# Performance work log

Hardware: AMD Instinct MI355X
Metric: run time of the kernel (lower is better)

## Reference

```python
import jax, jax.numpy as jnp
import numpy as np

ATTEN_SIZE = 5  # half-window; module-global atten_size in source (0 there is non-functional)
B, S, D_IN, HID, OUT = 8, 2048, 512, 512, 2


def _xavier(key, shape):
    fan_in, fan_out = shape
    std = (2.0 / (fan_in + fan_out)) ** 0.5
    return jax.random.normal(key, shape, dtype=jnp.float32) * std


def setup_inputs() -> dict:
    key = jax.random.key(0)
    ks = jax.random.split(key, 8)
    return {
        "x": jax.random.normal(ks[0], (B, S, D_IN), dtype=jnp.float32),
        "W1": _xavier(ks[1], (D_IN, HID)),
        "b1": jnp.zeros((1, 1, HID), dtype=jnp.float32),
        "Wq": _xavier(ks[2], (HID, HID)),
        "Wk": _xavier(ks[3], (HID, HID)),
        "Wv": _xavier(ks[4], (HID, HID)),
        "W2": _xavier(ks[5], (HID, HID)),
        "b2": jnp.zeros((1, 1, HID), dtype=jnp.float32),
        "Wfc": _xavier(ks[6], (HID, OUT)),
        "bfc": jnp.zeros((OUT,), dtype=jnp.float32),
    }


def reference(x, W1, b1, Wq, Wk, Wv, W2, b2, Wfc, bfc):
    A = ATTEN_SIZE
    Wn = 2 * A + 1
    h = jax.nn.relu(x @ W1 + b1)                      # [B,S,H]
    b, s, hd = h.shape
    padded = jnp.pad(h, ((0, 0), (A, A), (0, 0)))     # [B,S+2A,H]
    # torch pad+roll(k)+stack+slice equals reversed window: x_nei[p, j] = padded[p + 2A - j]
    idx = jnp.arange(s)[:, None] + (2 * A - jnp.arange(Wn))[None, :]  # [S,Wn]
    x_nei = padded[:, idx, :]                         # [B,S,Wn,H]
    q = h @ Wq                                        # [B,S,H]
    k = x_nei @ Wk                                    # [B,S,Wn,H]
    v = x_nei @ Wv                                    # [B,S,Wn,H]
    scale = jnp.asarray(np.sqrt(float(hd)), dtype=h.dtype)
    scores = jnp.einsum('bsh,bswh->bsw', q, k)[:, :, None, :] / scale  # [B,S,1,Wn]
    # Faithful to torch.nn.Softmax(dim=2) on a singleton dim -> all ones
    w = jax.nn.softmax(scores, axis=2)                # [B,S,1,Wn]
    aw = jnp.einsum('bsjw,bswh->bsjh', w, v).reshape(b, s, hd)  # [B,S,H]
    out = jax.nn.relu(aw @ W2 + b2) @ Wfc + bfc       # [B,S,OUT]
    return out, aw
```

## Files before the change

### kernel.cpp

```cpp
#include <hip/hip_runtime.h>
#include <stdint.h>

#define B_   8
#define S_   2048
#define HID_ 512
#define M_   (B_ * S_)
#define AW_  5

typedef __attribute__((ext_vector_type(8))) short bf16x8;
typedef __attribute__((ext_vector_type(4))) float f32x4;
typedef unsigned short u16;

__device__ __forceinline__ u16 f2bf(float f) {
    uint32_t u = __builtin_bit_cast(uint32_t, f);
    u += 0x7FFFu + ((u >> 16) & 1u);
    return (u16)(u >> 16);
}
__device__ __forceinline__ float bf2f(u16 h) {
    uint32_t u = ((uint32_t)h) << 16;
    return __builtin_bit_cast(float, u);
}

__device__ __forceinline__ void gload16(const void* g, void* l) {
    __builtin_amdgcn_global_load_lds(
        (const __attribute__((address_space(1))) void*)(uintptr_t)g,
        (__attribute__((address_space(3))) void*)(uint32_t)(uintptr_t)l,
        16, 0, 0);
}

__global__ __launch_bounds__(256) void conv_x(const float* __restrict__ x,
                                              u16* __restrict__ xb) {
    const long i = (long)(blockIdx.x * 256 + threadIdx.x) * 8;
    const float4 a = *(const float4*)&x[i];
    const float4 b = *(const float4*)&x[i + 4];
    union { u16 u[8]; int4 v; } r;
    r.u[0] = f2bf(a.x); r.u[1] = f2bf(a.y); r.u[2] = f2bf(a.z); r.u[3] = f2bf(a.w);
    r.u[4] = f2bf(b.x); r.u[5] = f2bf(b.y); r.u[6] = f2bf(b.z); r.u[7] = f2bf(b.w);
    *(int4*)&xb[i] = r.v;
}

__global__ __launch_bounds__(256) void trans_w(const float* __restrict__ W1,
                                               const float* __restrict__ Wv,
                                               const float* __restrict__ W2,
                                               u16* __restrict__ W1t,
                                               u16* __restrict__ Wvt,
                                               u16* __restrict__ W2t) {
    const float* src = blockIdx.z == 0 ? W1 : (blockIdx.z == 1 ? Wv : W2);
    u16* dst = blockIdx.z == 0 ? W1t : (blockIdx.z == 1 ? Wvt : W2t);
    __shared__ float tile[32][33];
    const int k0 = blockIdx.y * 32, n0 = blockIdx.x * 32;
    const int tr = threadIdx.x >> 5, tc = threadIdx.x & 31;
#pragma unroll
    for (int p = 0; p < 4; ++p)
        tile[tr + p * 8][tc] = src[(long)(k0 + tr + p * 8) * HID_ + n0 + tc];
    __syncthreads();
#pragma unroll
    for (int p = 0; p < 4; ++p)
        dst[(long)(n0 + tr + p * 8) * HID_ + k0 + tc] = f2bf(tile[tc][tr + p * 8]);
}

template <bool RELU, bool BIAS, bool F32OUT>
__global__ __launch_bounds__(256, 2) void gemm_bf16(const u16* __restrict__ A,
                                                    const u16* __restrict__ Bt,
                                                    const float* __restrict__ bias,
                                                    u16* __restrict__ C,
                                                    float* __restrict__ Cf) {
    __shared__ __attribute__((aligned(16))) u16 As[2][128 * 64];
    __shared__ __attribute__((aligned(16))) u16 Bs[2][128 * 64];

    const int tid = threadIdx.x;
    const int bid = blockIdx.x;
    const int swz = (bid & 7) * 64 + (bid >> 3);
    const int  bn   = (swz & 3) * 128;
    const long brow = (long)(swz >> 2) * 128;

    const int w  = tid >> 6;
    const int l  = tid & 63;
    const int wm = (w >> 1) * 64;
    const int wn = (w & 1) * 64;
    const int lr  = l & 15;
    const int lkb = (l >> 4) * 16;
    const int sw  = (lr & 7) << 4;

    int pq[4];
    const u16* srcA[4];
    const u16* srcB[4];
#pragma unroll
    for (int q = 0; q < 4; ++q) {
        const int p   = tid * 16 + q * 4096;
        const int row = p >> 7;
        const int cb  = (p & 127) ^ ((row & 7) << 4);
        pq[q]   = p;
        srcA[q] = A  + (brow + row) * 512 + (cb >> 1);
        srcB[q] = Bt + (long)(bn + row) * 512 + (cb >> 1);
    }

    f32x4 acc[4][4];
#pragma unroll
    for (int i = 0; i < 4; ++i)
#pragma unroll
        for (int j = 0; j < 4; ++j) {
            f32x4 z = {0.f, 0.f, 0.f, 0.f};
            acc[i][j] = z;
        }

#define STAGE(buf, k0)                                                   \
    {                                                                    \
        _Pragma("unroll") for (int q = 0; q < 4; ++q) {                  \
            gload16(srcA[q] + (k0), (char*)&As[buf][0] + pq[q]);         \
            gload16(srcB[q] + (k0), (char*)&Bs[buf][0] + pq[q]);         \
        }                                                                \
    }

    int cur = 0;
    STAGE(0, 0);
    __syncthreads();

    for (int t = 0; t < 8; ++t) {
        if (t < 7) STAGE(cur ^ 1, (t + 1) * 64);
#pragma unroll
        for (int kk = 0; kk < 2; ++kk) {
            bf16x8 af[4], bfr[4];
#pragma unroll
            for (int i = 0; i < 4; ++i) {
                const int off = (wm + i * 16 + lr) * 128 + ((kk * 64 + lkb) ^ sw);
                af[i] = *(const bf16x8*)((const char*)&As[cur][0] + off);
            }
#pragma unroll
            for (int j = 0; j < 4; ++j) {
                const int off = (wn + j * 16 + lr) * 128 + ((kk * 64 + lkb) ^ sw);
                bfr[j] = *(const bf16x8*)((const char*)&Bs[cur][0] + off);
            }
#pragma unroll
            for (int i = 0; i < 4; ++i)
#pragma unroll
                for (int j = 0; j < 4; ++j)
                    acc[i][j] = __builtin_amdgcn_mfma_f32_16x16x32_bf16(
                        af[i], bfr[j], acc[i][j], 0, 0, 0);
        }
        __syncthreads();
        cur ^= 1;
    }
#undef STAGE

    float bv[4];
    if (BIAS) {
#pragma unroll
        for (int j = 0; j < 4; ++j) bv[j] = bias[bn + wn + j * 16 + lr];
    }
    const int rq = (l >> 4) * 4;
#pragma unroll
    for (int i = 0; i < 4; ++i)
#pragma unroll
        for (int q = 0; q < 4; ++q) {
            const long row = brow + wm + i * 16 + rq + q;
            u16*   crow = C + row * 512 + bn + wn + lr;
            float* frow = F32OUT ? (Cf + row * 512 + bn + wn + lr) : nullptr;
#pragma unroll
            for (int j = 0; j < 4; ++j) {
                float v = acc[i][j][q];
                if (BIAS) v += bv[j];
                if (RELU) v = fmaxf(v, 0.f);
                crow[j * 16] = f2bf(v);
                if (F32OUT) frow[j * 16] = v;
            }
        }
}

__global__ __launch_bounds__(256) void winsum(const u16* __restrict__ h,
                                              u16* __restrict__ hs) {
    const long idx = (long)blockIdx.x * 256 + threadIdx.x;
    const int  c8  = (int)(idx & 63);
    const long bs  = idx >> 6;
    const int  s   = (int)(bs & (S_ - 1));

    float acc[8] = {};
#pragma unroll
    for (int d = -AW_; d <= AW_; ++d) {
        const int ss = s + d;
        if (0 <= ss && ss < S_) {
            const int4 v = *(const int4*)&h[(bs + d) * HID_ + c8 * 8];
            const u16* u = (const u16*)&v;
#pragma unroll
            for (int e = 0; e < 8; ++e) acc[e] += bf2f(u[e]);
        }
    }
    union { u16 u[8]; int4 v; } r;
#pragma unroll
    for (int e = 0; e < 8; ++e) r.u[e] = f2bf(acc[e]);
    *(int4*)&hs[bs * HID_ + c8 * 8] = r.v;
}

__global__ __launch_bounds__(256) void fc_out(const u16* __restrict__ t,
                                              const float* __restrict__ Wfc,
                                              const float* __restrict__ bfc,
                                              float* __restrict__ out) {
    const int row  = blockIdx.x * 4 + (threadIdx.x >> 6);
    const int lane = threadIdx.x & 63;

    float a0 = 0.f, a1 = 0.f;
    for (int i = lane; i < HID_; i += 64) {
        const float tv = bf2f(t[(long)row * HID_ + i]);
        a0 += tv * Wfc[2 * i];
        a1 += tv * Wfc[2 * i + 1];
    }
#pragma unroll
    for (int off = 32; off > 0; off >>= 1) {
        a0 += __shfl_down(a0, off);
        a1 += __shfl_down(a1, off);
    }
    if (lane == 0) {
        out[row * 2 + 0] = a0 + bfc[0];
        out[row * 2 + 1] = a1 + bfc[1];
    }
}

__global__ __launch_bounds__(256) void expand_aw(const u16* __restrict__ awb,
                                                 float* __restrict__ aw) {
    const long i = (long)(blockIdx.x * 256 + threadIdx.x) * 8;
    const int4 v = *(const int4*)&awb[i];
    const u16* u = (const u16*)&v;
    float4 o0 = {bf2f(u[0]), bf2f(u[1]), bf2f(u[2]), bf2f(u[3])};
    float4 o1 = {bf2f(u[4]), bf2f(u[5]), bf2f(u[6]), bf2f(u[7])};
    *(float4*)&aw[i]     = o0;
    *(float4*)&aw[i + 4] = o1;
}

extern "C" void kernel_launch(void* const* d_in, const int* in_sizes, int n_in,
                              void* d_out, int out_size, void* d_ws, size_t ws_size,
                              hipStream_t stream) {
    const float* x   = (const float*)d_in[0];
    const float* W1  = (const float*)d_in[1];
    const float* b1  = (const float*)d_in[2];
    const float* Wv  = (const float*)d_in[5];
    const float* W2  = (const float*)d_in[6];
    const float* b2  = (const float*)d_in[7];
    const float* Wfc = (const float*)d_in[8];
    const float* bfc = (const float*)d_in[9];

    float* out_part = (float*)d_out;
    float* aw_f32   = (float*)d_out + (long)M_ * 2;

    const size_t PEL = (size_t)M_ * HID_;
    unsigned char* ws = (unsigned char*)d_ws;

    u16* W1t = (u16*)aw_f32;
    u16* xb  = (u16*)aw_f32 + 8388608;

    const bool fuse = ws_size >= (size_t)(1 << 20) + 2 * PEL * sizeof(u16);
    u16 *Wvt, *W2t, *P0, *P1;
    if (fuse) {
        Wvt = (u16*)ws;
        W2t = Wvt + 262144;
        P0  = (u16*)(ws + (1 << 20));
        P1  = P0 + PEL;
    } else {
        Wvt = W1t + 262144;
        W2t = Wvt + 262144;
        P0  = (u16*)ws;
        P1  = P0 + PEL;
    }

    conv_x<<<4096, 256, 0, stream>>>(x, xb);
    trans_w<<<dim3(16, 16, 3), 256, 0, stream>>>(W1, Wv, W2, W1t, Wvt, W2t);
    gemm_bf16<true, true, false><<<512, 256, 0, stream>>>(xb, W1t, b1, P0, nullptr);
    winsum<<<4096, 256, 0, stream>>>(P0, P1);
    if (fuse)
        gemm_bf16<false, false, true><<<512, 256, 0, stream>>>(P1, Wvt, nullptr, P0, aw_f32);
    else
        gemm_bf16<false, false, false><<<512, 256, 0, stream>>>(P1, Wvt, nullptr, P0, nullptr);
    gemm_bf16<true, true, false><<<512, 256, 0, stream>>>(P0, W2t, b2, P1, nullptr);
    fc_out<<<M_ / 4, 256, 0, stream>>>(P1, Wfc, bfc, out_part);
    if (!fuse)
        expand_aw<<<4096, 256, 0, stream>>>(P0, aw_f32);
}
```

Baseline: 78.73 us.

## Fuse x conversion into GEMM1, reorder winsum after Wv, fuse fc into GEMM4

Removes the separate fp32-to-bf16 conversion of x by loading fp32 A tiles in the first GEMM and converting them in registers before the LDS write. It also applies the window sum after the Wv projection, which is valid because the projection is linear, and has that window-sum kernel write both the bf16 and fp32 attention output, so no separate expand pass is needed. The final 512x2 projection is folded into the W2 GEMM epilogue through per-column-slot partial sums plus a small reduction kernel. These changes cut several full-size intermediate passes. In exchange, GEMM1 now does synchronous global loads, and the workspace is aliased more aggressively (W2t is carved out of g after g is consumed).

```diff
diff --git a/kernel.cpp b/kernel.cpp
--- a/kernel.cpp
+++ b/kernel.cpp
@@ -28,25 +28,12 @@
         16, 0, 0);
 }
 
-__global__ __launch_bounds__(256) void conv_x(const float* __restrict__ x,
-                                              u16* __restrict__ xb) {
-    const long i = (long)(blockIdx.x * 256 + threadIdx.x) * 8;
-    const float4 a = *(const float4*)&x[i];
-    const float4 b = *(const float4*)&x[i + 4];
-    union { u16 u[8]; int4 v; } r;
-    r.u[0] = f2bf(a.x); r.u[1] = f2bf(a.y); r.u[2] = f2bf(a.z); r.u[3] = f2bf(a.w);
-    r.u[4] = f2bf(b.x); r.u[5] = f2bf(b.y); r.u[6] = f2bf(b.z); r.u[7] = f2bf(b.w);
-    *(int4*)&xb[i] = r.v;
-}
-
-__global__ __launch_bounds__(256) void trans_w(const float* __restrict__ W1,
-                                               const float* __restrict__ Wv,
-                                               const float* __restrict__ W2,
-                                               u16* __restrict__ W1t,
-                                               u16* __restrict__ Wvt,
-                                               u16* __restrict__ W2t) {
-    const float* src = blockIdx.z == 0 ? W1 : (blockIdx.z == 1 ? Wv : W2);
-    u16* dst = blockIdx.z == 0 ? W1t : (blockIdx.z == 1 ? Wvt : W2t);
+__global__ __launch_bounds__(256) void trans2w(const float* __restrict__ S0,
+                                               const float* __restrict__ S1,
+                                               u16* __restrict__ D0,
+                                               u16* __restrict__ D1) {
+    const float* src = blockIdx.z ? S1 : S0;
+    u16* dst = blockIdx.z ? D1 : D0;
     __shared__ float tile[32][33];
     const int k0 = blockIdx.y * 32, n0 = blockIdx.x * 32;
     const int tr = threadIdx.x >> 5, tc = threadIdx.x & 31;
@@ -59,12 +46,10 @@
         dst[(long)(n0 + tr + p * 8) * HID_ + k0 + tc] = f2bf(tile[tc][tr + p * 8]);
 }
 
-template <bool RELU, bool BIAS, bool F32OUT>
-__global__ __launch_bounds__(256, 2) void gemm_bf16(const u16* __restrict__ A,
-                                                    const u16* __restrict__ Bt,
-                                                    const float* __restrict__ bias,
-                                                    u16* __restrict__ C,
-                                                    float* __restrict__ Cf) {
+__global__ __launch_bounds__(256, 2) void gemm1_f32a(const float* __restrict__ A,
+                                                     const u16* __restrict__ Bt,
+                                                     const float* __restrict__ bias,
+                                                     u16* __restrict__ C) {
     __shared__ __attribute__((aligned(16))) u16 As[2][128 * 64];
     __shared__ __attribute__((aligned(16))) u16 Bs[2][128 * 64];
 
@@ -82,6 +67,143 @@
     const int lkb = (l >> 4) * 16;
     const int sw  = (lr & 7) << 4;
 
+    const int r0 = tid >> 2;
+    const int c0 = (tid & 3) * 16;
+    const int r1 = 64 + r0;
+    const float* ga0 = A + (brow + r0) * 512 + c0;
+    const float* ga1 = A + (brow + r1) * 512 + c0;
+    char* lw = (char*)&As[0][0];
+    const int wb00 = r0 * 128 + ((c0 * 2 +  0) ^ ((r0 & 7) << 4));
+    const int wb01 = r0 * 128 + ((c0 * 2 + 16) ^ ((r0 & 7) << 4));
+    const int wb10 = r1 * 128 + ((c0 * 2 +  0) ^ ((r1 & 7) << 4));
+    const int wb11 = r1 * 128 + ((c0 * 2 + 16) ^ ((r1 & 7) << 4));
+
+    int pq[4];
+    const u16* srcB[4];
+#pragma unroll
+    for (int q = 0; q < 4; ++q) {
+        const int p   = tid * 16 + q * 4096;
+        const int row = p >> 7;
+        const int cb  = (p & 127) ^ ((row & 7) << 4);
+        pq[q]   = p;
+        srcB[q] = Bt + (long)(bn + row) * 512 + (cb >> 1);
+    }
+
+    f32x4 acc[4][4];
+#pragma unroll
+    for (int i = 0; i < 4; ++i)
+#pragma unroll
+        for (int j = 0; j < 4; ++j) {
+            f32x4 z = {0.f, 0.f, 0.f, 0.f};
+            acc[i][j] = z;
+        }
+
+    float4 ra[4], rb[4];
+
+#define LOADA(k0)                                                        \
+    {                                                                    \
+        _Pragma("unroll") for (int u = 0; u < 4; ++u) {                  \
+            ra[u] = *(const float4*)(ga0 + (k0) + u * 4);                \
+            rb[u] = *(const float4*)(ga1 + (k0) + u * 4);                \
+        }                                                                \
+    }
+#define CVTWRITE(buf)                                                    \
+    {                                                                    \
+        union { u16 u[8]; int4 v; } q0, q1, q2, q3;                      \
+        q0.u[0]=f2bf(ra[0].x); q0.u[1]=f2bf(ra[0].y); q0.u[2]=f2bf(ra[0].z); q0.u[3]=f2bf(ra[0].w); \
+        q0.u[4]=f2bf(ra[1].x); q0.u[5]=f2bf(ra[1].y); q0.u[6]=f2bf(ra[1].z); q0.u[7]=f2bf(ra[1].w); \
+        q1.u[0]=f2bf(ra[2].x); q1.u[1]=f2bf(ra[2].y); q1.u[2]=f2bf(ra[2].z); q1.u[3]=f2bf(ra[2].w); \
+        q1.u[4]=f2bf(ra[3].x); q1.u[5]=f2bf(ra[3].y); q1.u[6]=f2bf(ra[3].z); q1.u[7]=f2bf(ra[3].w); \
+        q2.u[0]=f2bf(rb[0].x); q2.u[1]=f2bf(rb[0].y); q2.u[2]=f2bf(rb[0].z); q2.u[3]=f2bf(rb[0].w); \
+        q2.u[4]=f2bf(rb[1].x); q2.u[5]=f2bf(rb[1].y); q2.u[6]=f2bf(rb[1].z); q2.u[7]=f2bf(rb[1].w); \
+        q3.u[0]=f2bf(rb[2].x); q3.u[1]=f2bf(rb[2].y); q3.u[2]=f2bf(rb[2].z); q3.u[3]=f2bf(rb[2].w); \
+        q3.u[4]=f2bf(rb[3].x); q3.u[5]=f2bf(rb[3].y); q3.u[6]=f2bf(rb[3].z); q3.u[7]=f2bf(rb[3].w); \
+        *(int4*)(lw + (buf) * 16384 + wb00) = q0.v;                      \
+        *(int4*)(lw + (buf) * 16384 + wb01) = q1.v;                      \
+        *(int4*)(lw + (buf) * 16384 + wb10) = q2.v;                      \
+        *(int4*)(lw + (buf) * 16384 + wb11) = q3.v;                      \
+    }
+#define STAGEB(buf, k0)                                                  \
+    {                                                                    \
+        _Pragma("unroll") for (int q = 0; q < 4; ++q)                    \
+            gload16(srcB[q] + (k0), (char*)&Bs[buf][0] + pq[q]);         \
+    }
+
+    LOADA(0);
+    STAGEB(0, 0);
+    CVTWRITE(0);
+    __syncthreads();
+
+    int cur = 0;
+    for (int t = 0; t < 8; ++t) {
+        if (t < 7) {
+            LOADA((t + 1) * 64);
+            STAGEB(cur ^ 1, (t + 1) * 64);
+        }
+#pragma unroll
+        for (int kk = 0; kk < 2; ++kk) {
+            bf16x8 af[4], bfr[4];
+#pragma unroll
+            for (int i = 0; i < 4; ++i) {
+                const int off = (wm + i * 16 + lr) * 128 + ((kk * 64 + lkb) ^ sw);
+                af[i] = *(const bf16x8*)((const char*)&As[cur][0] + off);
+            }
+#pragma unroll
+            for (int j = 0; j < 4; ++j) {
+                const int off = (wn + j * 16 + lr) * 128 + ((kk * 64 + lkb) ^ sw);
+                bfr[j] = *(const bf16x8*)((const char*)&Bs[cur][0] + off);
+            }
+#pragma unroll
+            for (int i = 0; i < 4; ++i)
+#pragma unroll
+                for (int j = 0; j < 4; ++j)
+                    acc[i][j] = __builtin_amdgcn_mfma_f32_16x16x32_bf16(
+                        af[i], bfr[j], acc[i][j], 0, 0, 0);
+        }
+        if (t < 7) CVTWRITE(cur ^ 1);
+        __syncthreads();
+        cur ^= 1;
+    }
+#undef LOADA
+#undef CVTWRITE
+#undef STAGEB
+
+    float bv[4];
+#pragma unroll
+    for (int j = 0; j < 4; ++j) bv[j] = bias[bn + wn + j * 16 + lr];
+    const int rq = (l >> 4) * 4;
+#pragma unroll
+    for (int i = 0; i < 4; ++i)
+#pragma unroll
+        for (int q = 0; q < 4; ++q) {
+            const long row = brow + wm + i * 16 + rq + q;
+            u16* crow = C + row * 512 + bn + wn + lr;
+#pragma unroll
+            for (int j = 0; j < 4; ++j)
+                crow[j * 16] = f2bf(fmaxf(acc[i][j][q] + bv[j], 0.f));
+        }
+}
+
+__global__ __launch_bounds__(256, 2) void gemm_bf16(const u16* __restrict__ A,
+                                                    const u16* __restrict__ Bt,
+                                                    u16* __restrict__ C) {
+    __shared__ __attribute__((aligned(16))) u16 As[2][128 * 64];
+    __shared__ __attribute__((aligned(16))) u16 Bs[2][128 * 64];
+
+    const int tid = threadIdx.x;
+    const int bid = blockIdx.x;
+    const int swz = (bid & 7) * 64 + (bid >> 3);
+    const int  bn   = (swz & 3) * 128;
+    const long brow = (long)(swz >> 2) * 128;
+
+    const int w  = tid >> 6;
+    const int l  = tid & 63;
+    const int wm = (w >> 1) * 64;
+    const int wn = (w & 1) * 64;
+    const int lr  = l & 15;
+    const int lkb = (l >> 4) * 16;
+    const int sw  = (lr & 7) << 4;
+
     int pq[4];
     const u16* srcA[4];
     const u16* srcB[4];
@@ -143,32 +265,140 @@
     }
 #undef STAGE
 
-    float bv[4];
-    if (BIAS) {
-#pragma unroll
-        for (int j = 0; j < 4; ++j) bv[j] = bias[bn + wn + j * 16 + lr];
-    }
     const int rq = (l >> 4) * 4;
 #pragma unroll
     for (int i = 0; i < 4; ++i)
 #pragma unroll
         for (int q = 0; q < 4; ++q) {
             const long row = brow + wm + i * 16 + rq + q;
-            u16*   crow = C + row * 512 + bn + wn + lr;
-            float* frow = F32OUT ? (Cf + row * 512 + bn + wn + lr) : nullptr;
+            u16* crow = C + row * 512 + bn + wn + lr;
+#pragma unroll
+            for (int j = 0; j < 4; ++j)
+                crow[j * 16] = f2bf(acc[i][j][q]);
+        }
+}
+
+__global__ __launch_bounds__(256, 2) void gemm4_fc(const u16* __restrict__ A,
+                                                   const u16* __restrict__ Bt,
+                                                   const float* __restrict__ b2,
+                                                   const float* __restrict__ Wfc,
+                                                   float* __restrict__ partials) {
+    __shared__ __attribute__((aligned(16))) u16 As[2][128 * 64];
+    __shared__ __attribute__((aligned(16))) u16 Bs[2][128 * 64];
+
+    const int tid = threadIdx.x;
+    const int bid = blockIdx.x;
+    const int swz = (bid & 7) * 64 + (bid >> 3);
+    const int  bn   = (swz & 3) * 128;
+    const long brow = (long)(swz >> 2) * 128;
+
+    const int w  = tid >> 6;
+    const int l  = tid & 63;
+    const int wm = (w >> 1) * 64;
+    const int wn = (w & 1) * 64;
+    const int lr  = l & 15;
+    const int lkb = (l >> 4) * 16;
+    const int sw  = (lr & 7) << 4;
+
+    int pq[4];
+    const u16* srcA[4];
+    const u16* srcB[4];
+#pragma unroll
+    for (int q = 0; q < 4; ++q) {
+        const int p   = tid * 16 + q * 4096;
+        const int row = p >> 7;
+        const int cb  = (p & 127) ^ ((row & 7) << 4);
+        pq[q]   = p;
+        srcA[q] = A  + (brow + row) * 512 + (cb >> 1);
+        srcB[q] = Bt + (long)(bn + row) * 512 + (cb >> 1);
+    }
+
+    f32x4 acc[4][4];
+#pragma unroll
+    for (int i = 0; i < 4; ++i)
+#pragma unroll
+        for (int j = 0; j < 4; ++j) {
+            f32x4 z = {0.f, 0.f, 0.f, 0.f};
+            acc[i][j] = z;
+        }
+
+#define STAGE(buf, k0)                                                   \
+    {                                                                    \
+        _Pragma("unroll") for (int q = 0; q < 4; ++q) {                  \
+            gload16(srcA[q] + (k0), (char*)&As[buf][0] + pq[q]);         \
+            gload16(srcB[q] + (k0), (char*)&Bs[buf][0] + pq[q]);         \
+        }                                                                \
+    }
+
+    int cur = 0;
+    STAGE(0, 0);
+    __syncthreads();
+
+    for (int t = 0; t < 8; ++t) {
+        if (t < 7) STAGE(cur ^ 1, (t + 1) * 64);
+#pragma unroll
+        for (int kk = 0; kk < 2; ++kk) {
+            bf16x8 af[4], bfr[4];
+#pragma unroll
+            for (int i = 0; i < 4; ++i) {
+                const int off = (wm + i * 16 + lr) * 128 + ((kk * 64 + lkb) ^ sw);
+                af[i] = *(const bf16x8*)((const char*)&As[cur][0] + off);
+            }
 #pragma unroll
             for (int j = 0; j < 4; ++j) {
-                float v = acc[i][j][q];
-                if (BIAS) v += bv[j];
-                if (RELU) v = fmaxf(v, 0.f);
-                crow[j * 16] = f2bf(v);
-                if (F32OUT) frow[j * 16] = v;
-            }
-        }
-}
-
-__global__ __launch_bounds__(256) void winsum(const u16* __restrict__ h,
-                                              u16* __restrict__ hs) {
+                const int off = (wn + j * 16 + lr) * 128 + ((kk * 64 + lkb) ^ sw);
+                bfr[j] = *(const bf16x8*)((const char*)&Bs[cur][0] + off);
+            }
+#pragma unroll
+            for (int i = 0; i < 4; ++i)
+#pragma unroll
+                for (int j = 0; j < 4; ++j)
+                    acc[i][j] = __builtin_amdgcn_mfma_f32_16x16x32_bf16(
+                        af[i], bfr[j], acc[i][j], 0, 0, 0);
+        }
+        __syncthreads();
+        cur ^= 1;
+    }
+#undef STAGE
+
+    float bv[4], w0[4], w1[4];
+#pragma unroll
+    for (int j = 0; j < 4; ++j) {
+        const int col = bn + wn + j * 16 + lr;
+        bv[j] = b2[col];
+        w0[j] = Wfc[2 * col];
+        w1[j] = Wfc[2 * col + 1];
+    }
+    const int rq = (l >> 4) * 4;
+    const int slot = (bn >> 7) * 2 + (wn >> 6);
+#pragma unroll
+    for (int i = 0; i < 4; ++i)
+#pragma unroll
+        for (int q = 0; q < 4; ++q) {
+            float s0 = 0.f, s1 = 0.f;
+#pragma unroll
+            for (int j = 0; j < 4; ++j) {
+                const float v = fmaxf(acc[i][j][q] + bv[j], 0.f);
+                s0 += v * w0[j];
+                s1 += v * w1[j];
+            }
+#pragma unroll
+            for (int m = 1; m < 16; m <<= 1) {
+                s0 += __shfl_xor(s0, m);
+                s1 += __shfl_xor(s1, m);
+            }
+            if (lr == 0) {
+                const long row = brow + wm + i * 16 + rq + q;
+                float* pp = partials + ((long)slot * M_ + row) * 2;
+                pp[0] = s0;
+                pp[1] = s1;
+            }
+        }
+}
+
+__global__ __launch_bounds__(256) void winsum_f(const u16* __restrict__ g,
+                                                u16* __restrict__ awb,
+                                                float* __restrict__ awf) {
     const long idx = (long)blockIdx.x * 256 + threadIdx.x;
     const int  c8  = (int)(idx & 63);
     const long bs  = idx >> 6;
@@ -179,7 +409,7 @@
     for (int d = -AW_; d <= AW_; ++d) {
         const int ss = s + d;
         if (0 <= ss && ss < S_) {
-            const int4 v = *(const int4*)&h[(bs + d) * HID_ + c8 * 8];
+            const int4 v = *(const int4*)&g[(bs + d) * HID_ + c8 * 8];
             const u16* u = (const u16*)&v;
 #pragma unroll
             for (int e = 0; e < 8; ++e) acc[e] += bf2f(u[e]);
@@ -188,42 +418,25 @@
     union { u16 u[8]; int4 v; } r;
 #pragma unroll
     for (int e = 0; e < 8; ++e) r.u[e] = f2bf(acc[e]);
-    *(int4*)&hs[bs * HID_ + c8 * 8] = r.v;
-}
-
-__global__ __launch_bounds__(256) void fc_out(const u16* __restrict__ t,
-                                              const float* __restrict__ Wfc,
-                                              const float* __restrict__ bfc,
-                                              float* __restrict__ out) {
-    const int row  = blockIdx.x * 4 + (threadIdx.x >> 6);
-    const int lane = threadIdx.x & 63;
-
-    float a0 = 0.f, a1 = 0.f;
-    for (int i = lane; i < HID_; i += 64) {
-        const float tv = bf2f(t[(long)row * HID_ + i]);
-        a0 += tv * Wfc[2 * i];
-        a1 += tv * Wfc[2 * i + 1];
-    }
-#pragma unroll
-    for (int off = 32; off > 0; off >>= 1) {
-        a0 += __shfl_down(a0, off);
-        a1 += __shfl_down(a1, off);
-    }
-    if (lane == 0) {
-        out[row * 2 + 0] = a0 + bfc[0];
-        out[row * 2 + 1] = a1 + bfc[1];
-    }
-}
-
-__global__ __launch_bounds__(256) void expand_aw(const u16* __restrict__ awb,
-                                                 float* __restrict__ aw) {
-    const long i = (long)(blockIdx.x * 256 + threadIdx.x) * 8;
-    const int4 v = *(const int4*)&awb[i];
-    const u16* u = (const u16*)&v;
-    float4 o0 = {bf2f(u[0]), bf2f(u[1]), bf2f(u[2]), bf2f(u[3])};
-    float4 o1 = {bf2f(u[4]), bf2f(u[5]), bf2f(u[6]), bf2f(u[7])};
-    *(float4*)&aw[i]     = o0;
-    *(float4*)&aw[i + 4] = o1;
+    *(int4*)&awb[bs * HID_ + c8 * 8] = r.v;
+    float4 o0 = {acc[0], acc[1], acc[2], acc[3]};
+    float4 o1 = {acc[4], acc[5], acc[6], acc[7]};
+    *(float4*)&awf[bs * HID_ + c8 * 8]     = o0;
+    *(float4*)&awf[bs * HID_ + c8 * 8 + 4] = o1;
+}
+
+__global__ __launch_bounds__(256) void fc_reduce(const float* __restrict__ partials,
+                                                 const float* __restrict__ bfc,
+                                                 float* __restrict__ out) {
+    const int row = blockIdx.x * 256 + threadIdx.x;
+    float s0 = bfc[0], s1 = bfc[1];
+#pragma unroll
+    for (int p = 0; p < 8; ++p) {
+        s0 += partials[((long)p * M_ + row) * 2 + 0];
+        s1 += partials[((long)p * M_ + row) * 2 + 1];
+    }
+    out[row * 2 + 0] = s0;
+    out[row * 2 + 1] = s1;
 }
 
 extern "C" void kernel_launch(void* const* d_in, const int* in_sizes, int n_in,
@@ -241,36 +454,20 @@
     float* out_part = (float*)d_out;
     float* aw_f32   = (float*)d_out + (long)M_ * 2;
 
-    const size_t PEL = (size_t)M_ * HID_;
-    unsigned char* ws = (unsigned char*)d_ws;
-
     u16* W1t = (u16*)aw_f32;
-    u16* xb  = (u16*)aw_f32 + 8388608;
-
-    const bool fuse = ws_size >= (size_t)(1 << 20) + 2 * PEL * sizeof(u16);
-    u16 *Wvt, *W2t, *P0, *P1;
-    if (fuse) {
-        Wvt = (u16*)ws;
-        W2t = Wvt + 262144;
-        P0  = (u16*)(ws + (1 << 20));
-        P1  = P0 + PEL;
-    } else {
-        Wvt = W1t + 262144;
-        W2t = Wvt + 262144;
-        P0  = (u16*)ws;
-        P1  = P0 + PEL;
-    }
-
-    conv_x<<<4096, 256, 0, stream>>>(x, xb);
-    trans_w<<<dim3(16, 16, 3), 256, 0, stream>>>(W1, Wv, W2, W1t, Wvt, W2t);
-    gemm_bf16<true, true, false><<<512, 256, 0, stream>>>(xb, W1t, b1, P0, nullptr);
-    winsum<<<4096, 256, 0, stream>>>(P0, P1);
-    if (fuse)
-        gemm_bf16<false, false, true><<<512, 256, 0, stream>>>(P1, Wvt, nullptr, P0, aw_f32);
-    else
-        gemm_bf16<false, false, false><<<512, 256, 0, stream>>>(P1, Wvt, nullptr, P0, nullptr);
-    gemm_bf16<true, true, false><<<512, 256, 0, stream>>>(P0, W2t, b2, P1, nullptr);
-    fc_out<<<M_ / 4, 256, 0, stream>>>(P1, Wfc, bfc, out_part);
-    if (!fuse)
-        expand_aw<<<4096, 256, 0, stream>>>(P0, aw_f32);
-}
+    u16* Wvt = W1t + 262144;
+
+    u16* h   = (u16*)d_ws;
+    u16* g   = (u16*)d_ws + 8388608;
+    u16* awb = h;
+    u16* W2t = g;
+    float* partials = (float*)((char*)d_ws + 16 * 1024 * 1024 + 512 * 1024);
+
+    trans2w<<<dim3(16, 16, 2), 256, 0, stream>>>(W1, Wv, W1t, Wvt);
+    gemm1_f32a<<<512, 256, 0, stream>>>(x, W1t, b1, h);
+    gemm_bf16<<<512, 256, 0, stream>>>(h, Wvt, g);
+    winsum_f<<<4096, 256, 0, stream>>>(g, awb, aw_f32);
+    trans2w<<<dim3(16, 16, 1), 256, 0, stream>>>(W2, W2, W2t, W2t);
+    gemm4_fc<<<512, 256, 0, stream>>>(awb, W2t, b2, Wfc, partials);
+    fc_reduce<<<64, 256, 0, stream>>>(partials, bfc, out_part);
+}
```

Result: no change. 78.79 us (+0.1%).
